# Optimization experiments

Hardware: AMD Instinct MI355X
Metric: run time of the kernel (lower is better)

The kernel has to match this reference:

```python
import jax, jax.numpy as jnp
import numpy as np
from jax import lax

B, N, C = 8, 16384, 128
HEADS, FF, KS = 8, 3.0, 5
HD = C // HEADS

def setup_inputs() -> dict:
    key = jax.random.key(0)
    ks = jax.random.split(key, 10)
    r = lambda k, s, sc=0.02: jax.random.normal(k, s, dtype=jnp.float32) * sc
    return {
        "x": jax.random.normal(ks[0], (B, N, C), dtype=jnp.float32),
        "Wq": r(ks[1], (C, C)),
        "Wkv": r(ks[2], (C, C)),
        "Wproj": r(ks[3], (C, C)),
        "bproj": jnp.zeros((C,), jnp.float32),
        "w_g": jax.random.normal(ks[4], (C, 1), dtype=jnp.float32),
        "scale": r(ks[5], (1, 1, C), 0.1),
        "pos_enc": r(ks[6], (1, N, C), 0.02),
        "dwc_w": r(ks[7], (HD, 1, KS, KS), 0.1),
        "dwc_b": jnp.zeros((HD,), jnp.float32),
        "H": 128,
        "W": 128,
    }

def _l2(a, axis):
    return jnp.sqrt(jnp.sum(a * a, axis=axis, keepdims=True))

def reference(x, Wq, Wkv, Wproj, bproj, w_g, scale, pos_enc, dwc_w, dwc_b, H, W):
    b, n_tok, c = x.shape
    scale_factor = HD ** (-0.5)
    q = x @ Wq.T                      # (B,N,C)
    k = x @ Wkv.T + pos_enc           # (B,N,C)  sr_ratio=1 path
    s = jax.nn.softplus(scale)
    q = (jax.nn.relu(q) + 1e-6) / s
    k = (jax.nn.relu(k) + 1e-6) / s
    qn, kn = _l2(q, -1), _l2(k, -1)
    q = q ** FF
    k = k ** FF
    q = q / _l2(q, -1) * qn
    k = k / _l2(k, -1) * kn
    A = (q @ w_g) * scale_factor      # (B,N,1)
    A = A / jnp.maximum(_l2(A, 1), 1e-12)  # F.normalize over dim=1
    G = jnp.sum(A * q, axis=1)        # (B,C)
    xg = G[:, None, :] * k            # (B,N,C)
    qh = q.reshape(b, n_tok, HEADS, HD).transpose(0, 2, 1, 3)  # (B,h,N,d)
    kh = k.reshape(b, n_tok, HEADS, HD).transpose(0, 2, 1, 3)
    z = 1.0 / (jnp.einsum('bhnd,bhd->bhn', qh, kh.mean(axis=2)) + 1e-6)
    xh = xg.reshape(b, n_tok, HEADS, HD).transpose(0, 2, 1, 3) * z[..., None]
    xo = xh.transpose(0, 2, 1, 3).reshape(b, n_tok, c)
    # faithful second transpose+reshape (memory reinterpretation in the source)
    xo = xo.transpose(0, 2, 1).reshape(b, n_tok, c)
    kimg = kh.reshape(b * HEADS, H, W, HD).transpose(0, 3, 1, 2)  # (B*h,d,H,W)
    pad = KS // 2
    conv = lax.conv_general_dilated(kimg, dwc_w, (1, 1), [(pad, pad), (pad, pad)],
                                    dimension_numbers=('NCHW', 'OIHW', 'NCHW'),
                                    feature_group_count=HD)
    conv = conv + dwc_b[None, :, None, None]
    xo = xo + conv.reshape(b, c, n_tok).transpose(0, 2, 1)
    return xo @ Wproj.T + bproj
```

## Files before the change

### kernel.cpp

```cpp
#include <hip/hip_runtime.h>
#include <hip/hip_bf16.h>

#define BB 8
#define NN 16384
#define CC 128

typedef __attribute__((ext_vector_type(8))) short bf16x8;
typedef __attribute__((ext_vector_type(4))) short short4v;
typedef __attribute__((ext_vector_type(4))) float f32x4;

__device__ __forceinline__ unsigned short f2bf(float f) {
    union { float f; unsigned u; } v; v.f = f;
    unsigned r = v.u + 0x7fffu + ((v.u >> 16) & 1u);
    return (unsigned short)(r >> 16);
}
__device__ __forceinline__ float bf2f(unsigned short h) {
    union { unsigned u; float f; } v; v.u = ((unsigned)h) << 16;
    return v.f;
}
__device__ __forceinline__ void split_trunc(float f, short& hi, short& lo) {
    union { float f; unsigned u; } v; v.f = f;
    const unsigned short hu = (unsigned short)(v.u >> 16);
    union { unsigned u; float f; } hf; hf.u = ((unsigned)hu) << 16;
    union { float f; unsigned u; } r; r.f = f - hf.f;
    hi = (short)hu;
    lo = (short)(r.u >> 16);
}

__global__ __launch_bounds__(256) void wprep_kernel(
    const float* __restrict__ Wq, const float* __restrict__ Wkv,
    const float* __restrict__ Wp, const float* __restrict__ scale,
    unsigned short* __restrict__ whi, unsigned short* __restrict__ wlo,
    float* __restrict__ sps)
{
    const int bid = blockIdx.x;
    if (bid == 48) {
        if (threadIdx.x < 128)
            sps[threadIdx.x] = 1.f / log1pf(expf(scale[threadIdx.x]));
        return;
    }
    const int mat = bid >> 4;
    const float* src = (mat == 0) ? Wq : ((mat == 1) ? Wkv : Wp);
    const int off = (bid & 15) * 1024 + threadIdx.x * 4;
    const float4 v = *(const float4*)(src + off);
    float f[4] = {v.x, v.y, v.z, v.w};
    short4v hv, lv;
#pragma unroll
    for (int j = 0; j < 4; ++j) {
        short h, lo2;
        split_trunc(f[j], h, lo2);
        hv[j] = h; lv[j] = lo2;
    }
    *(short4v*)(whi + mat * 16384 + off) = hv;
    *(short4v*)(wlo + mat * 16384 + off) = lv;
}

__global__ __launch_bounds__(256, 1) void qk_mfma_kernel(
    const float* __restrict__ x, const unsigned short* __restrict__ whi,
    const unsigned short* __restrict__ wlo, const float* __restrict__ w_g,
    const float* __restrict__ sps, const float* __restrict__ pos_enc,
    unsigned short* __restrict__ qout, unsigned short* __restrict__ kout,
    unsigned short* __restrict__ ktout, float* __restrict__ partial)
{
    __shared__ __align__(16) char wsm[131072];
    __shared__ float wpart[4][257];
    __shared__ float apl[128];

    const int tid  = threadIdx.x;
    const int w    = tid >> 6;
    const int l    = tid & 63;
    const int blk  = blockIdx.x;
    const int tok0 = blk * 128;
    const int tokb = (blk & 127) * 128;

    bf16x8 xh[2][4], xl[2][4];
#pragma unroll
    for (int n = 0; n < 2; ++n) {
        const int r = w * 32 + n * 16 + (l & 15);
        const float* rowp = x + (tok0 + r) * 128 + (l >> 4) * 8;
#pragma unroll
        for (int kt = 0; kt < 4; ++kt) {
            const f32x4 a = *(const f32x4*)(rowp + kt * 32);
            const f32x4 b = *(const f32x4*)(rowp + kt * 32 + 4);
            const float f[8] = {a[0], a[1], a[2], a[3], b[0], b[1], b[2], b[3]};
            bf16x8 hv, lv;
#pragma unroll
            for (int j = 0; j < 8; ++j) {
                short h, lo2;
                split_trunc(f[j], h, lo2);
                hv[j] = h; lv[j] = lo2;
            }
            xh[n][kt] = hv; xl[n][kt] = lv;
        }
    }

#pragma unroll
    for (int it = 0; it < 32; ++it) {
        const int flat = it * 256 + tid;
        const int arr  = flat >> 11;
        const int c    = (flat >> 4) & 127;
        const int g    = flat & 15;
        const unsigned short* src = ((arr & 1) ? wlo : whi)
                                  + ((arr >> 1) ? 16384 : 0) + c * 128 + g * 8;
        const int dst = arr * 32768 + c * 256 + ((g * 16) ^ ((c & 7) << 4));
        *(bf16x8*)(wsm + dst) = *(const bf16x8*)src;
    }
    __syncthreads();

    const int crow = (l >> 4) * 4;
    f32x4 accq[8][2], acck[8][2];
#pragma unroll
    for (int m = 0; m < 8; ++m)
#pragma unroll
        for (int n = 0; n < 2; ++n) { accq[m][n] = (f32x4)0.f; acck[m][n] = (f32x4)0.f; }

#pragma unroll
    for (int m = 0; m < 8; ++m) {
        const int c = m * 16 + (l & 15);
        const int sw = (c & 7) << 4;
        bf16x8 aqh[4], aql[4], akh[4], akl[4];
#pragma unroll
        for (int kt = 0; kt < 4; ++kt) {
            const int fo = c * 256 + ((kt * 64 + (l >> 4) * 16) ^ sw);
            aqh[kt] = *(const bf16x8*)(wsm + fo);
            aql[kt] = *(const bf16x8*)(wsm + 32768 + fo);
            akh[kt] = *(const bf16x8*)(wsm + 65536 + fo);
            akl[kt] = *(const bf16x8*)(wsm + 98304 + fo);
        }
#pragma unroll
        for (int n = 0; n < 2; ++n)
#pragma unroll
            for (int kt = 0; kt < 4; ++kt) {
                accq[m][n] = __builtin_amdgcn_mfma_f32_16x16x32_bf16(aqh[kt], xh[n][kt], accq[m][n], 0, 0, 0);
                acck[m][n] = __builtin_amdgcn_mfma_f32_16x16x32_bf16(akh[kt], xh[n][kt], acck[m][n], 0, 0, 0);
                accq[m][n] = __builtin_amdgcn_mfma_f32_16x16x32_bf16(aqh[kt], xl[n][kt], accq[m][n], 0, 0, 0);
                acck[m][n] = __builtin_amdgcn_mfma_f32_16x16x32_bf16(akh[kt], xl[n][kt], acck[m][n], 0, 0, 0);
                accq[m][n] = __builtin_amdgcn_mfma_f32_16x16x32_bf16(aql[kt], xh[n][kt], accq[m][n], 0, 0, 0);
                acck[m][n] = __builtin_amdgcn_mfma_f32_16x16x32_bf16(akl[kt], xh[n][kt], acck[m][n], 0, 0, 0);
            }
    }
    __syncthreads();

    {
#pragma unroll
        for (int m = 0; m < 8; ++m) {
            const float4 is4 = *(const float4*)(sps + m * 16 + crow);
            const float is[4] = {is4.x, is4.y, is4.z, is4.w};
#pragma unroll
            for (int n = 0; n < 2; ++n)
#pragma unroll
                for (int j = 0; j < 4; ++j)
                    accq[m][n][j] = (fmaxf(accq[m][n][j], 0.f) + 1e-6f) * is[j];
        }
        float fqn[2];
#pragma unroll
        for (int n = 0; n < 2; ++n) {
            float s2 = 0.f, s6 = 0.f;
#pragma unroll
            for (int m = 0; m < 8; ++m)
#pragma unroll
                for (int j = 0; j < 4; ++j) {
                    const float v = accq[m][n][j], v2 = v * v;
                    s2 += v2; s6 += v2 * v2 * v2;
                }
            s2 += __shfl_xor(s2, 16); s6 += __shfl_xor(s6, 16);
            s2 += __shfl_xor(s2, 32); s6 += __shfl_xor(s6, 32);
            fqn[n] = sqrtf(s2 / s6);
        }
#pragma unroll
        for (int m = 0; m < 8; ++m)
#pragma unroll
            for (int n = 0; n < 2; ++n)
#pragma unroll
                for (int j = 0; j < 4; ++j) {
                    const float v = accq[m][n][j];
                    accq[m][n][j] = v * v * v * fqn[n];
                }
        float d0 = 0.f, d1 = 0.f;
#pragma unroll
        for (int m = 0; m < 8; ++m) {
            const float4 wgv = *(const float4*)(w_g + m * 16 + crow);
#pragma unroll
            for (int j = 0; j < 4; ++j) {
                const float wg = (j == 0) ? wgv.x : (j == 1) ? wgv.y : (j == 2) ? wgv.z : wgv.w;
                d0 += accq[m][0][j] * wg;
                d1 += accq[m][1][j] * wg;
            }
        }
        d0 += __shfl_xor(d0, 16); d0 += __shfl_xor(d0, 32);
        d1 += __shfl_xor(d1, 16); d1 += __shfl_xor(d1, 32);
        const float ap0 = 0.25f * d0, ap1 = 0.25f * d1;

        float ssa = ap0 * ap0 + ap1 * ap1;
        ssa += __shfl_xor(ssa, 1); ssa += __shfl_xor(ssa, 2);
        ssa += __shfl_xor(ssa, 4); ssa += __shfl_xor(ssa, 8);
        if (l == 0) wpart[w][256] = ssa;
        if (l < 16) { apl[w * 32 + l] = ap0; apl[w * 32 + 16 + l] = ap1; }

        float g4[4] = {0.f, 0.f, 0.f, 0.f};
#pragma unroll
        for (int n = 0; n < 2; ++n) {
            const int t = l & 15;
            const int rb = w * 8192 + t * 512;
#pragma unroll
            for (int m = 0; m < 8; ++m) {
                const int ad = rb + (((m * 16 + crow) * 4) ^ ((t & 7) << 4));
                *(f32x4*)(wsm + ad) = accq[m][n];
            }
            asm volatile("s_waitcnt lgkmcnt(0)" ::: "memory");
#pragma unroll
            for (int j = 0; j < 8; ++j) {
                const int fid = j * 64 + l;
                const int row = fid >> 5;
                const int c4  = fid & 31;
                const int rb3 = w * 8192 + row * 512;
                const f32x4 v = *(f32x4*)(wsm + rb3 + ((c4 * 16) ^ ((row & 7) << 4)));
                const float apv = apl[w * 32 + n * 16 + row];
                short4v qv;
#pragma unroll
                for (int i = 0; i < 4; ++i) {
                    g4[i] += apv * v[i];
                    qv[i] = (short)f2bf(v[i]);
                }
                *(short4v*)(qout + (tok0 + w * 32 + n * 16 + row) * 128 + c4 * 4) = qv;
            }
        }
#pragma unroll
        for (int i = 0; i < 4; ++i) g4[i] += __shfl_xor(g4[i], 32);
        if (l < 32) {
#pragma unroll
            for (int i = 0; i < 4; ++i) wpart[w][(l & 31) * 4 + i] = g4[i];
        }
    }

    {
#pragma unroll
        for (int m = 0; m < 8; ++m) {
            const float4 is4 = *(const float4*)(sps + m * 16 + crow);
            const float is[4] = {is4.x, is4.y, is4.z, is4.w};
#pragma unroll
            for (int n = 0; n < 2; ++n) {
                const int t = tokb + w * 32 + n * 16 + (l & 15);
                const float4 p = *(const float4*)(pos_enc + t * 128 + m * 16 + crow);
                const float pe[4] = {p.x, p.y, p.z, p.w};
#pragma unroll
                for (int j = 0; j < 4; ++j)
                    acck[m][n][j] = (fmaxf(acck[m][n][j] + pe[j], 0.f) + 1e-6f) * is[j];
            }
        }
        float fkn[2];
#pragma unroll
        for (int n = 0; n < 2; ++n) {
            float s2 = 0.f, s6 = 0.f;
#pragma unroll
            for (int m = 0; m < 8; ++m)
#pragma unroll
                for (int j = 0; j < 4; ++j) {
                    const float v = acck[m][n][j], v2 = v * v;
                    s2 += v2; s6 += v2 * v2 * v2;
                }
            s2 += __shfl_xor(s2, 16); s6 += __shfl_xor(s6, 16);
            s2 += __shfl_xor(s2, 32); s6 += __shfl_xor(s6, 32);
            fkn[n] = sqrtf(s2 / s6);
        }
#pragma unroll
        for (int m = 0; m < 8; ++m)
#pragma unroll
            for (int n = 0; n < 2; ++n)
#pragma unroll
                for (int j = 0; j < 4; ++j) {
                    const float v = acck[m][n][j];
                    acck[m][n][j] = v * v * v * fkn[n];
                }
        float ks4[4] = {0.f, 0.f, 0.f, 0.f};
#pragma unroll
        for (int n = 0; n < 2; ++n) {
            const int t = l & 15;
            const int rb = w * 8192 + t * 512;
#pragma unroll
            for (int m = 0; m < 8; ++m) {
                const int ad = rb + (((m * 16 + crow) * 4) ^ ((t & 7) << 4));
                *(f32x4*)(wsm + ad) = acck[m][n];
            }
            asm volatile("s_waitcnt lgkmcnt(0)" ::: "memory");
#pragma unroll
            for (int j = 0; j < 8; ++j) {
                const int fid = j * 64 + l;
                const int row = fid >> 5;
                const int c4  = fid & 31;
                const int rb3 = w * 8192 + row * 512;
                const f32x4 v = *(f32x4*)(wsm + rb3 + ((c4 * 16) ^ ((row & 7) << 4)));
                short4v kv;
#pragma unroll
                for (int i = 0; i < 4; ++i) {
                    ks4[i] += v[i];
                    kv[i] = (short)f2bf(v[i]);
                }
                *(short4v*)(kout + (tok0 + w * 32 + n * 16 + row) * 128 + c4 * 4) = kv;
            }
        }
#pragma unroll
        for (int i = 0; i < 4; ++i) ks4[i] += __shfl_xor(ks4[i], 32);
        if (l < 32) {
#pragma unroll
            for (int i = 0; i < 4; ++i) wpart[w][128 + (l & 31) * 4 + i] = ks4[i];
        }
    }

    __syncthreads();
#pragma unroll
    for (int m = 0; m < 8; ++m)
#pragma unroll
        for (int n = 0; n < 2; ++n)
#pragma unroll
            for (int j = 0; j < 4; ++j) {
                const int ch = m * 16 + crow + j;
                const int tl = w * 32 + n * 16 + (l & 15);
                *(unsigned short*)(wsm + ch * 264 + tl * 2) = f2bf(acck[m][n][j]);
            }
    __syncthreads();
    {
        const int bb = blk >> 7;
        unsigned* ktp = (unsigned*)ktout;
#pragma unroll
        for (int it = 0; it < 32; ++it) {
            const int idx = it * 256 + tid;
            const int row = idx >> 6;
            const int col = idx & 63;
            const unsigned v = *(unsigned*)(wsm + row * 264 + col * 4);
            ktp[(size_t)(bb * 128 + row) * 8192 + (blk & 127) * 64 + col] = v;
        }
    }

    __syncthreads();
    float* pblk = partial + blk * 257;
    if (tid < 128) {
        pblk[tid] = wpart[0][tid] + wpart[1][tid] + wpart[2][tid] + wpart[3][tid];
        pblk[128 + tid] = wpart[0][128 + tid] + wpart[1][128 + tid] +
                          wpart[2][128 + tid] + wpart[3][128 + tid];
    } else if (tid == 128) {
        pblk[256] = wpart[0][256] + wpart[1][256] + wpart[2][256] + wpart[3][256];
    }
}

__global__ __launch_bounds__(256) void reduce_kernel(
    const float* __restrict__ partial, float* __restrict__ G,
    float* __restrict__ kbar)
{
    const int b = blockIdx.x;
    const int tid = threadIdx.x;
    __shared__ float tmp[4];

    float ssa = (tid < 128) ? partial[(b * 128 + tid) * 257 + 256] : 0.f;
#pragma unroll
    for (int o = 32; o >= 1; o >>= 1) ssa += __shfl_xor(ssa, o);
    if ((tid & 63) == 0) tmp[tid >> 6] = ssa;
    __syncthreads();
    const float anorm = fmaxf(sqrtf(tmp[0] + tmp[1] + tmp[2] + tmp[3]), 1e-12f);
    const float inv_a = 1.f / anorm;

    if (tid < 128) {
        float g = 0.f;
        for (int t = 0; t < 128; ++t)
            g += partial[(b * 128 + t) * 257 + tid];
        G[b * 128 + tid] = g * inv_a;
    } else {
        const int c2 = tid - 128;
        float s = 0.f;
        for (int t = 0; t < 128; ++t)
            s += partial[(b * 128 + t) * 257 + 128 + c2];
        kbar[b * 128 + c2] = s * (1.f / 16384.f);
    }
}

__global__ __launch_bounds__(256) void z_kernel(
    const unsigned short* __restrict__ q, const float* __restrict__ kbar,
    float* __restrict__ z)
{
    const int bid = blockIdx.x;
    const int b   = bid >> 8;
    const int tg  = bid & 255;
    const int tid = threadIdx.x;
    const int t   = tid >> 2;
    const int qt  = tid & 3;
    const int tok = tg * 64 + t;

    const unsigned short* qp = q + ((size_t)b * NN + tok) * 128 + qt * 32;
    const float* kb = kbar + b * 128 + qt * 32;

    float dot0 = 0.f, dot1 = 0.f;
#pragma unroll
    for (int c = 0; c < 4; ++c) {
        const short4v q4a = *(const short4v*)(qp + c * 8);
        const short4v q4b = *(const short4v*)(qp + c * 8 + 4);
        const float4 k4a = *(const float4*)(kb + c * 8);
        const float4 k4b = *(const float4*)(kb + c * 8 + 4);
        float d = bf2f((unsigned short)q4a[0]) * k4a.x + bf2f((unsigned short)q4a[1]) * k4a.y +
                  bf2f((unsigned short)q4a[2]) * k4a.z + bf2f((unsigned short)q4a[3]) * k4a.w +
                  bf2f((unsigned short)q4b[0]) * k4b.x + bf2f((unsigned short)q4b[1]) * k4b.y +
                  bf2f((unsigned short)q4b[2]) * k4b.z + bf2f((unsigned short)q4b[3]) * k4b.w;
        if (c < 2) dot0 += d; else dot1 += d;
    }
    z[((size_t)b * 8 + qt * 2) * NN + tok]     = 1.f / (dot0 + 1e-6f);
    z[((size_t)b * 8 + qt * 2 + 1) * NN + tok] = 1.f / (dot1 + 1e-6f);
}

__global__ __launch_bounds__(256, 3) void scp_kernel(
    float* __restrict__ out, const unsigned short* __restrict__ kbuf,
    const unsigned short* __restrict__ kt, const float* __restrict__ z,
    const float* __restrict__ G,
    const unsigned short* __restrict__ whi, const unsigned short* __restrict__ wlo,
    const float* __restrict__ bp, const float* __restrict__ dwc_w,
    const float* __restrict__ dwc_b)
{
    __shared__ __align__(16) char smem[32768];
    __shared__ float wct[25][16];
    __shared__ float bi[16];
    __shared__ float Gs;

    const int tid  = threadIdx.x;
    const int bid0 = blockIdx.x;
    const int bid  = (bid0 & 7) * 128 + (bid0 >> 3);
    const int cc   = bid & 127;
    const int b    = bid >> 7;
    const int n0   = bid * 128;

    for (int i = tid; i < 400; i += 256)
        wct[i >> 4][i & 15] = dwc_w[(i & 15) * 25 + (i >> 4)];
    if (tid < 16) bi[tid] = dwc_b[tid];
    if (tid == 0) Gs = G[b * 128 + cc];
    __syncthreads();

    const int l  = tid & 31;
    const int xg = tid >> 5;
    const int dbase = (l & 3) * 4;

    const float Gcc = Gs;
    const unsigned short* kub = kt + ((size_t)b * 128 + cc) * NN;
    const float* zr = z + ((size_t)b * 8 + (cc >> 4)) * NN;
    const float4 b4 = *(const float4*)(&bi[dbase]);
    const float bv[4] = {b4.x, b4.y, b4.z, b4.w};

#pragma unroll
    for (int h = 0; h < 2; ++h) {
        float4 acc[8];
#pragma unroll
        for (int i = 0; i < 8; ++i) acc[i] = make_float4(0.f, 0.f, 0.f, 0.f);

#pragma unroll
        for (int dy = 0; dy < 5; ++dy) {
            const int yy = cc + dy - 2;
            if (yy < 0 || yy > 127) continue;
            const unsigned short* rowb = kbuf + (b * NN + yy * 128) * CC + l * 4;
            float4 rowv[12];
#pragma unroll
            for (int xi = 0; xi < 12; ++xi) {
                const int xx = xg * 16 + h * 8 - 2 + xi;
                if (xx >= 0 && xx < 128) {
                    const short4v kv4 = *(const short4v*)(rowb + xx * CC);
                    rowv[xi] = make_float4(bf2f((unsigned short)kv4[0]),
                                           bf2f((unsigned short)kv4[1]),
                                           bf2f((unsigned short)kv4[2]),
                                           bf2f((unsigned short)kv4[3]));
                } else {
                    rowv[xi] = make_float4(0.f, 0.f, 0.f, 0.f);
                }
            }
#pragma unroll
            for (int dx = 0; dx < 5; ++dx) {
                const float4 wv = *(const float4*)(&wct[dy * 5 + dx][dbase]);
#pragma unroll
                for (int i = 0; i < 8; ++i) {
                    acc[i].x += wv.x * rowv[i + dx].x;
                    acc[i].y += wv.y * rowv[i + dx].y;
                    acc[i].z += wv.z * rowv[i + dx].z;
                    acc[i].w += wv.w * rowv[i + dx].w;
                }
            }
        }

#pragma unroll
        for (int i = 0; i < 8; ++i) {
            const int r = xg * 16 + h * 8 + i;
            const int toks = r * 128 + l * 4;
            const short4v ku4 = *(const short4v*)(kub + toks);
            const float4 z4 = *(const float4*)(zr + toks);
            const float zz[4] = {z4.x, z4.y, z4.z, z4.w};
            const float av[4] = {acc[i].x, acc[i].y, acc[i].z, acc[i].w};
            short4v hv;
#pragma unroll
            for (int c = 0; c < 4; ++c) {
                const float f = Gcc * bf2f((unsigned short)ku4[c]) * zz[c] + av[c] + bv[c];
                hv[c] = (short)f2bf(f);
            }
            const int ad = r * 256 + (((l >> 1) * 16) ^ ((r & 7) << 4)) + (l & 1) * 8;
            *(short4v*)(smem + ad) = hv;
        }
    }
    __syncthreads();

    const int w  = tid >> 6;
    const int ll = tid & 63;
    bf16x8 xh[2][4];
    {
        const int lg16 = (ll >> 4) * 16;
#pragma unroll
        for (int n = 0; n < 2; ++n) {
            const int r = w * 32 + n * 16 + (ll & 15);
            const int rb = r * 256;
            const int sw = (r & 7) << 4;
#pragma unroll
            for (int kt2 = 0; kt2 < 4; ++kt2)
                xh[n][kt2] = *(bf16x8*)(smem + rb + ((kt2 * 64 + lg16) ^ sw));
        }
    }
    const int crow = (ll >> 4) * 4;
    f32x4 pacc[8][2];
#pragma unroll
    for (int m = 0; m < 8; ++m)
#pragma unroll
        for (int n = 0; n < 2; ++n) pacc[m][n] = (f32x4)0.f;

#pragma unroll
    for (int m = 0; m < 8; ++m) {
        const int c = m * 16 + (ll & 15);
        bf16x8 ah[4], al[4];
#pragma unroll
        for (int kt2 = 0; kt2 < 4; ++kt2) {
            const int off = 32768 + c * 128 + kt2 * 32 + (ll >> 4) * 8;
            ah[kt2] = *(const bf16x8*)(whi + off);
            al[kt2] = *(const bf16x8*)(wlo + off);
        }
#pragma unroll
        for (int n = 0; n < 2; ++n)
#pragma unroll
            for (int kt2 = 0; kt2 < 4; ++kt2) {
                pacc[m][n] = __builtin_amdgcn_mfma_f32_16x16x32_bf16(ah[kt2], xh[n][kt2], pacc[m][n], 0, 0, 0);
                pacc[m][n] = __builtin_amdgcn_mfma_f32_16x16x32_bf16(al[kt2], xh[n][kt2], pacc[m][n], 0, 0, 0);
            }
    }

#pragma unroll
    for (int m = 0; m < 8; ++m) {
        const float4 bq = *(const float4*)(bp + m * 16 + crow);
        const float bb[4] = {bq.x, bq.y, bq.z, bq.w};
#pragma unroll
        for (int n = 0; n < 2; ++n)
#pragma unroll
            for (int j = 0; j < 4; ++j) pacc[m][n][j] += bb[j];
    }
    __syncthreads();
#pragma unroll
    for (int n = 0; n < 2; ++n) {
        const int t = ll & 15;
        const int rb = w * 8192 + t * 512;
#pragma unroll
        for (int m = 0; m < 8; ++m) {
            const int ad = rb + (((m * 16 + crow) * 4) ^ ((t & 7) << 4));
            *(f32x4*)(smem + ad) = pacc[m][n];
        }
        asm volatile("s_waitcnt lgkmcnt(0)" ::: "memory");
#pragma unroll
        for (int j = 0; j < 8; ++j) {
            const int fid = j * 64 + ll;
            const int row = fid >> 5;
            const int c4  = fid & 31;
            const int rb3 = w * 8192 + row * 512;
            const f32x4 v = *(f32x4*)(smem + rb3 + ((c4 * 16) ^ ((row & 7) << 4)));
            *(f32x4*)(out + (n0 + w * 32 + n * 16 + row) * 128 + c4 * 4) = v;
        }
    }
}

extern "C" void kernel_launch(void* const* d_in, const int* in_sizes, int n_in,
                              void* d_out, int out_size, void* d_ws, size_t ws_size,
                              hipStream_t stream)
{
    const float* x       = (const float*)d_in[0];
    const float* Wq      = (const float*)d_in[1];
    const float* Wkv     = (const float*)d_in[2];
    const float* Wproj   = (const float*)d_in[3];
    const float* bproj   = (const float*)d_in[4];
    const float* w_g     = (const float*)d_in[5];
    const float* scale   = (const float*)d_in[6];
    const float* pos_enc = (const float*)d_in[7];
    const float* dwc_w   = (const float*)d_in[8];
    const float* dwc_b   = (const float*)d_in[9];
    float* out = (float*)d_out;

    char* ws = (char*)d_ws;
    unsigned short* qbuf = (unsigned short*)(ws);
    unsigned short* kbuf = (unsigned short*)(ws + 33554432);
    unsigned short* ktbuf= (unsigned short*)(ws + 67108864);
    float* partial = (float*)(ws + 100663296);
    float* G       = (float*)(ws + 101715968);
    float* kbar    = (float*)(ws + 101720064);
    unsigned short* whi = (unsigned short*)(ws + 101724160);
    unsigned short* wlo = (unsigned short*)(ws + 101822464);
    float* sps     = (float*)(ws + 101920768);
    float* zbuf    = (float*)(ws + 101921280);

    wprep_kernel<<<dim3(49), dim3(256), 0, stream>>>(
        Wq, Wkv, Wproj, scale, whi, wlo, sps);
    qk_mfma_kernel<<<dim3(1024), dim3(256), 0, stream>>>(
        x, whi, wlo, w_g, sps, pos_enc, qbuf, kbuf, ktbuf, partial);
    reduce_kernel<<<dim3(8), dim3(256), 0, stream>>>(partial, G, kbar);
    z_kernel<<<dim3(2048), dim3(256), 0, stream>>>(qbuf, kbar, zbuf);
    scp_kernel<<<dim3(1024), dim3(256), 0, stream>>>(
        out, kbuf, ktbuf, zbuf, G, whi, wlo, bproj, dwc_w, dwc_b);
}
```

Baseline: 194.9 us.

## Drop token-major K buffer and compute depthwise conv from channel-major K

```diff
diff --git a/kernel.cpp b/kernel.cpp
--- a/kernel.cpp
+++ b/kernel.cpp
@@ -59,8 +59,8 @@
     const float* __restrict__ x, const unsigned short* __restrict__ whi,
     const unsigned short* __restrict__ wlo, const float* __restrict__ w_g,
     const float* __restrict__ sps, const float* __restrict__ pos_enc,
-    unsigned short* __restrict__ qout, unsigned short* __restrict__ kout,
-    unsigned short* __restrict__ ktout, float* __restrict__ partial)
+    unsigned short* __restrict__ qout, unsigned short* __restrict__ ktout,
+    float* __restrict__ partial)
 {
     __shared__ __align__(16) char wsm[131072];
     __shared__ float wpart[4][257];
@@ -272,39 +272,15 @@
                     const float v = acck[m][n][j];
                     acck[m][n][j] = v * v * v * fkn[n];
                 }
-        float ks4[4] = {0.f, 0.f, 0.f, 0.f};
-#pragma unroll
-        for (int n = 0; n < 2; ++n) {
-            const int t = l & 15;
-            const int rb = w * 8192 + t * 512;
-#pragma unroll
-            for (int m = 0; m < 8; ++m) {
-                const int ad = rb + (((m * 16 + crow) * 4) ^ ((t & 7) << 4));
-                *(f32x4*)(wsm + ad) = acck[m][n];
-            }
-            asm volatile("s_waitcnt lgkmcnt(0)" ::: "memory");
-#pragma unroll
-            for (int j = 0; j < 8; ++j) {
-                const int fid = j * 64 + l;
-                const int row = fid >> 5;
-                const int c4  = fid & 31;
-                const int rb3 = w * 8192 + row * 512;
-                const f32x4 v = *(f32x4*)(wsm + rb3 + ((c4 * 16) ^ ((row & 7) << 4)));
-                short4v kv;
-#pragma unroll
-                for (int i = 0; i < 4; ++i) {
-                    ks4[i] += v[i];
-                    kv[i] = (short)f2bf(v[i]);
-                }
-                *(short4v*)(kout + (tok0 + w * 32 + n * 16 + row) * 128 + c4 * 4) = kv;
-            }
-        }
-#pragma unroll
-        for (int i = 0; i < 4; ++i) ks4[i] += __shfl_xor(ks4[i], 32);
-        if (l < 32) {
-#pragma unroll
-            for (int i = 0; i < 4; ++i) wpart[w][128 + (l & 31) * 4 + i] = ks4[i];
-        }
+#pragma unroll
+        for (int m = 0; m < 8; ++m)
+#pragma unroll
+            for (int j = 0; j < 4; ++j) {
+                float s = acck[m][0][j] + acck[m][1][j];
+                s += __shfl_xor(s, 1); s += __shfl_xor(s, 2);
+                s += __shfl_xor(s, 4); s += __shfl_xor(s, 8);
+                if ((l & 15) == 0) wpart[w][128 + m * 16 + crow + j] = s;
+            }
     }
 
     __syncthreads();
@@ -405,10 +381,9 @@
     z[((size_t)b * 8 + qt * 2 + 1) * NN + tok] = 1.f / (dot1 + 1e-6f);
 }
 
-__global__ __launch_bounds__(256, 3) void scp_kernel(
-    float* __restrict__ out, const unsigned short* __restrict__ kbuf,
-    const unsigned short* __restrict__ kt, const float* __restrict__ z,
-    const float* __restrict__ G,
+__global__ __launch_bounds__(256, 2) void scp_kernel(
+    float* __restrict__ out, const unsigned short* __restrict__ kt,
+    const float* __restrict__ z, const float* __restrict__ G,
     const unsigned short* __restrict__ whi, const unsigned short* __restrict__ wlo,
     const float* __restrict__ bp, const float* __restrict__ dwc_w,
     const float* __restrict__ dwc_b)
@@ -431,71 +406,72 @@
     if (tid == 0) Gs = G[b * 128 + cc];
     __syncthreads();
 
-    const int l  = tid & 31;
-    const int xg = tid >> 5;
-    const int dbase = (l & 3) * 4;
+    const int ch4 = tid >> 3;
+    const int xg  = tid & 7;
+
+    float acc[4][16];
+#pragma unroll
+    for (int c = 0; c < 4; ++c)
+#pragma unroll
+        for (int i = 0; i < 16; ++i) acc[c][i] = 0.f;
+
+#pragma unroll
+    for (int dy = 0; dy < 5; ++dy) {
+        const int yy = cc + dy - 2;
+        if (yy < 0 || yy > 127) continue;
+#pragma unroll
+        for (int c = 0; c < 4; ++c) {
+            const int ch = ch4 * 4 + c;
+            const unsigned short* rowp = kt + ((size_t)b * 128 + ch) * NN
+                                            + yy * 128 + xg * 16 - 8;
+            float wf[32];
+#pragma unroll
+            for (int q4 = 0; q4 < 4; ++q4) {
+                const bf16x8 v = *(const bf16x8*)(rowp + q4 * 8);
+#pragma unroll
+                for (int e = 0; e < 8; ++e)
+                    wf[q4 * 8 + e] = bf2f((unsigned short)v[e]);
+            }
+            if (xg == 0) {
+#pragma unroll
+                for (int e = 0; e < 8; ++e) wf[e] = 0.f;
+            }
+            if (xg == 7) {
+#pragma unroll
+                for (int e = 24; e < 32; ++e) wf[e] = 0.f;
+            }
+            const int d = ch & 15;
+#pragma unroll
+            for (int dx = 0; dx < 5; ++dx) {
+                const float wv = wct[dy * 5 + dx][d];
+#pragma unroll
+                for (int i = 0; i < 16; ++i)
+                    acc[c][i] += wv * wf[i + dx + 6];
+            }
+        }
+    }
 
     const float Gcc = Gs;
     const unsigned short* kub = kt + ((size_t)b * 128 + cc) * NN;
     const float* zr = z + ((size_t)b * 8 + (cc >> 4)) * NN;
+    const int dbase = (ch4 & 3) * 4;
     const float4 b4 = *(const float4*)(&bi[dbase]);
     const float bv[4] = {b4.x, b4.y, b4.z, b4.w};
-
-#pragma unroll
-    for (int h = 0; h < 2; ++h) {
-        float4 acc[8];
-#pragma unroll
-        for (int i = 0; i < 8; ++i) acc[i] = make_float4(0.f, 0.f, 0.f, 0.f);
-
-#pragma unroll
-        for (int dy = 0; dy < 5; ++dy) {
-            const int yy = cc + dy - 2;
-            if (yy < 0 || yy > 127) continue;
-            const unsigned short* rowb = kbuf + (b * NN + yy * 128) * CC + l * 4;
-            float4 rowv[12];
-#pragma unroll
-            for (int xi = 0; xi < 12; ++xi) {
-                const int xx = xg * 16 + h * 8 - 2 + xi;
-                if (xx >= 0 && xx < 128) {
-                    const short4v kv4 = *(const short4v*)(rowb + xx * CC);
-                    rowv[xi] = make_float4(bf2f((unsigned short)kv4[0]),
-                                           bf2f((unsigned short)kv4[1]),
-                                           bf2f((unsigned short)kv4[2]),
-                                           bf2f((unsigned short)kv4[3]));
-                } else {
-                    rowv[xi] = make_float4(0.f, 0.f, 0.f, 0.f);
-                }
-            }
-#pragma unroll
-            for (int dx = 0; dx < 5; ++dx) {
-                const float4 wv = *(const float4*)(&wct[dy * 5 + dx][dbase]);
-#pragma unroll
-                for (int i = 0; i < 8; ++i) {
-                    acc[i].x += wv.x * rowv[i + dx].x;
-                    acc[i].y += wv.y * rowv[i + dx].y;
-                    acc[i].z += wv.z * rowv[i + dx].z;
-                    acc[i].w += wv.w * rowv[i + dx].w;
-                }
-            }
-        }
-
-#pragma unroll
-        for (int i = 0; i < 8; ++i) {
-            const int r = xg * 16 + h * 8 + i;
-            const int toks = r * 128 + l * 4;
-            const short4v ku4 = *(const short4v*)(kub + toks);
-            const float4 z4 = *(const float4*)(zr + toks);
-            const float zz[4] = {z4.x, z4.y, z4.z, z4.w};
-            const float av[4] = {acc[i].x, acc[i].y, acc[i].z, acc[i].w};
-            short4v hv;
-#pragma unroll
-            for (int c = 0; c < 4; ++c) {
-                const float f = Gcc * bf2f((unsigned short)ku4[c]) * zz[c] + av[c] + bv[c];
-                hv[c] = (short)f2bf(f);
-            }
-            const int ad = r * 256 + (((l >> 1) * 16) ^ ((r & 7) << 4)) + (l & 1) * 8;
-            *(short4v*)(smem + ad) = hv;
-        }
+#pragma unroll
+    for (int i = 0; i < 16; ++i) {
+        const int r = xg * 16 + i;
+        const int toks = r * 128 + ch4 * 4;
+        const short4v ku4 = *(const short4v*)(kub + toks);
+        const float4 z4 = *(const float4*)(zr + toks);
+        const float zz[4] = {z4.x, z4.y, z4.z, z4.w};
+        short4v hv;
+#pragma unroll
+        for (int c = 0; c < 4; ++c) {
+            const float f = Gcc * bf2f((unsigned short)ku4[c]) * zz[c] + acc[c][i] + bv[c];
+            hv[c] = (short)f2bf(f);
+        }
+        const int ad = r * 256 + (((ch4 >> 1) * 16) ^ ((r & 7) << 4)) + (ch4 & 1) * 8;
+        *(short4v*)(smem + ad) = hv;
     }
     __syncthreads();
 
@@ -590,22 +566,21 @@
 
     char* ws = (char*)d_ws;
     unsigned short* qbuf = (unsigned short*)(ws);
-    unsigned short* kbuf = (unsigned short*)(ws + 33554432);
-    unsigned short* ktbuf= (unsigned short*)(ws + 67108864);
-    float* partial = (float*)(ws + 100663296);
-    float* G       = (float*)(ws + 101715968);
-    float* kbar    = (float*)(ws + 101720064);
-    unsigned short* whi = (unsigned short*)(ws + 101724160);
-    unsigned short* wlo = (unsigned short*)(ws + 101822464);
-    float* sps     = (float*)(ws + 101920768);
-    float* zbuf    = (float*)(ws + 101921280);
+    unsigned short* ktbuf= (unsigned short*)(ws + 33554432);
+    float* partial = (float*)(ws + 67108864);
+    float* G       = (float*)(ws + 68161536);
+    float* kbar    = (float*)(ws + 68165632);
+    unsigned short* whi = (unsigned short*)(ws + 68169728);
+    unsigned short* wlo = (unsigned short*)(ws + 68268032);
+    float* sps     = (float*)(ws + 68366336);
+    float* zbuf    = (float*)(ws + 68366848);
 
     wprep_kernel<<<dim3(49), dim3(256), 0, stream>>>(
         Wq, Wkv, Wproj, scale, whi, wlo, sps);
     qk_mfma_kernel<<<dim3(1024), dim3(256), 0, stream>>>(
-        x, whi, wlo, w_g, sps, pos_enc, qbuf, kbuf, ktbuf, partial);
+        x, whi, wlo, w_g, sps, pos_enc, qbuf, ktbuf, partial);
     reduce_kernel<<<dim3(8), dim3(256), 0, stream>>>(partial, G, kbar);
     z_kernel<<<dim3(2048), dim3(256), 0, stream>>>(qbuf, kbar, zbuf);
     scp_kernel<<<dim3(1024), dim3(256), 0, stream>>>(
-        out, kbuf, ktbuf, zbuf, G, whi, wlo, bproj, dwc_w, dwc_b);
-}
+        out, ktbuf, zbuf, G, whi, wlo, bproj, dwc_w, dwc_b);
+}
```

New measurement: 181.0 us. 7.1% less time.
